# Kernel tuning notes

Hardware: AMD Instinct MI355X
Metric: run time of the kernel (lower is better)

The kernel has to match this reference:

```python
import jax, jax.numpy as jnp
import numpy as np

D_MODEL = 1024
N_HEADS = 16
HEAD_DIM = D_MODEL // N_HEADS
NEG_INF = -1e30


def _rotary(v):
    # v: [B, H, T, hd]. Original module rotates each (even, odd) pair by 90 deg:
    # out[..., 2i] = -v[..., 2i+1]; out[..., 2i+1] = v[..., 2i]
    v2 = v.reshape(*v.shape[:-1], HEAD_DIM // 2, 2)
    return jnp.stack([-v2[..., 1], v2[..., 0]], axis=-1).reshape(v.shape)


def setup_inputs() -> dict:
    key = jax.random.key(0)
    ks = jax.random.split(key, 9)
    B, T, D = 2, 2048, D_MODEL
    s = 1.0 / np.sqrt(D)
    inp = {
        "x": jax.random.normal(ks[0], (B, T, D), dtype=jnp.float32),
        "Wq_w": jax.random.normal(ks[1], (D, D), dtype=jnp.float32) * s,
        "Wq_b": jnp.zeros((D,), dtype=jnp.float32),
        "Wk_w": jax.random.normal(ks[2], (D, D), dtype=jnp.float32) * s,
        "Wk_b": jnp.zeros((D,), dtype=jnp.float32),
        "Wv_w": jax.random.normal(ks[3], (D, D), dtype=jnp.float32) * s,
        "Wv_b": jnp.zeros((D,), dtype=jnp.float32),
        "Wo_w": jax.random.normal(ks[4], (D, D), dtype=jnp.float32) * s,
        "Wo_b": jnp.zeros((D,), dtype=jnp.float32),
    }
    # create_sparse_mask: block-diagonal True windows of size T//4
    window = T // 4
    blk = jnp.arange(T) // window
    inp["sparse_mask"] = blk[:, None] == blk[None, :]
    return inp


def reference(x, Wq_w, Wq_b, Wk_w, Wk_b, Wv_w, Wv_b, Wo_w, Wo_b, sparse_mask):
    B, T, D = x.shape
    H, hd = N_HEADS, HEAD_DIM

    def proj(w, b):  # [B,T,D] -> [B,H,T,hd]
        return (x @ w.T + b).reshape(B, T, H, hd).transpose(0, 2, 1, 3)

    q = _rotary(proj(Wq_w, Wq_b))
    k = _rotary(proj(Wk_w, Wk_b))
    v = proj(Wv_w, Wv_b)

    scores = jnp.einsum("bhqd,bhkd->bhqk", q, k) / jnp.sqrt(jnp.asarray(hd, x.dtype))
    causal = jnp.tril(jnp.ones((T, T), dtype=bool))
    allowed = sparse_mask & causal  # block-diagonal AND causal
    scores = jnp.where(allowed, scores, NEG_INF)
    attn = jax.nn.softmax(scores, axis=-1)  # dropout_p=0.1 omitted (eval mode)
    out = jnp.einsum("bhqk,bhkd->bhqd", attn, v)
    out = out.transpose(0, 2, 1, 3).reshape(B, T, D)
    return out @ Wo_w.T + Wo_b
```

## Files before the change

### kernel.cpp

```cpp
#include <hip/hip_runtime.h>
#include <hip/hip_bf16.h>
#include <stdint.h>

typedef __attribute__((ext_vector_type(4))) float f32x4;
typedef __attribute__((ext_vector_type(8))) __bf16 bf16x8;
typedef __attribute__((ext_vector_type(4))) unsigned short u16x4;
typedef __attribute__((ext_vector_type(8))) unsigned short u16x8;
typedef const __attribute__((address_space(1))) void* as1_cvp;
typedef __attribute__((address_space(3))) void* as3_vp;

#define LOG2E 1.44269504088896340736f

#define VMW0() asm volatile("s_waitcnt vmcnt(0)" ::: "memory")
#define VMW2() asm volatile("s_waitcnt vmcnt(2)" ::: "memory")
#define VMW4() asm volatile("s_waitcnt vmcnt(4)" ::: "memory")
#define BAR()  do { __builtin_amdgcn_sched_barrier(0); __builtin_amdgcn_s_barrier(); \
                    __builtin_amdgcn_sched_barrier(0); } while (0)

static __device__ __forceinline__ unsigned short f2bf(float f) {
  union { float f; unsigned int u; } c; c.f = f;
  unsigned int r = c.u + 0x7FFFu + ((c.u >> 16) & 1u);
  return (unsigned short)(r >> 16);
}

static __device__ __forceinline__ void gl_lds16(const void* g, void* l) {
  __builtin_amdgcn_global_load_lds((as1_cvp)(uintptr_t)g, (as3_vp)(uintptr_t)l, 16, 0, 0);
}

__global__ __launch_bounds__(256) void cvt_kernel(
    const float* __restrict__ x, const float* __restrict__ wq, const float* __restrict__ wk,
    const float* __restrict__ wv, const float* __restrict__ wo,
    unsigned short* __restrict__ xb, unsigned short* __restrict__ wqb,
    unsigned short* __restrict__ wkb, unsigned short* __restrict__ wvb,
    unsigned short* __restrict__ wob) {
  long e = ((long)blockIdx.x * 256 + threadIdx.x) * 8;
  const float* s; unsigned short* d; long o;
  if (e < 4194304)      { s = x;  d = xb;  o = e; }
  else if (e < 5242880) { s = wq; d = wqb; o = e - 4194304; }
  else if (e < 6291456) { s = wk; d = wkb; o = e - 5242880; }
  else if (e < 7340032) { s = wv; d = wvb; o = e - 6291456; }
  else                  { s = wo; d = wob; o = e - 7340032; }
  float4 a = *(const float4*)(s + o);
  float4 b = *(const float4*)(s + o + 4);
  u16x8 v;
  v[0] = f2bf(a.x); v[1] = f2bf(a.y); v[2] = f2bf(a.z); v[3] = f2bf(a.w);
  v[4] = f2bf(b.x); v[5] = f2bf(b.y); v[6] = f2bf(b.z); v[7] = f2bf(b.w);
  *(u16x8*)(d + o) = v;
}

__global__ __launch_bounds__(512, 2) void gemm_qkv8(
    const unsigned short* __restrict__ xb, const unsigned short* __restrict__ wcat,
    const float* __restrict__ bq, const float* __restrict__ bk, const float* __restrict__ bv,
    unsigned short* __restrict__ qo, unsigned short* __restrict__ ko,
    unsigned short* __restrict__ vto) {
  __shared__ __align__(16) char lds[114688];
  const int tid = threadIdx.x;
  const int lane = tid & 63, wid = tid >> 6;
  const int wm = wid >> 1, wn = wid & 1;
  const int c = lane & 15, g = lane >> 4;

  const int bid = blockIdx.x;
  const int xcd = bid & 7, idx = bid >> 3;
  const int m0 = (((xcd >> 1) << 2) + (idx >> 3)) << 8;
  const int n0 = (((xcd & 1) << 3) + (idx & 7)) * 192;

  const int srow = tid >> 3;
  const int coff = (((tid & 7) ^ (srow & 7)) << 4);
  const char* Ab = (const char*)xb;
  const char* Bb = (const char*)wcat;

  const int swzr0 = ((g ^ (c & 7)) << 4);
  const int swzr1 = (((4 | g) ^ (c & 7)) << 4);

  f32x4 acc[4][6] = {};

  auto STAGE = [&](int kt, int unit) {
    char* db = lds + (kt & 1) * 57344;
    const char* gp; char* dst;
    if (unit < 3) {
      gp = Bb + ((long)(n0 + unit * 64 + srow) << 11) + (kt << 7) + coff;
      dst = db + 32768 + unit * 8192 + tid * 16;
    } else {
      const int u = unit - 3;
      gp = Ab + ((long)(m0 + u * 64 + srow) << 11) + (kt << 7) + coff;
      dst = db + u * 8192 + tid * 16;
    }
    gl_lds16(gp, dst);
  };

#pragma unroll
  for (int uu = 0; uu < 7; ++uu) STAGE(0, uu);
  VMW0();
  BAR();

#pragma unroll 1
  for (int kt = 0; kt < 16; ++kt) {
    const int bufb = (kt & 1) * 57344;
    if (kt < 15) {
#pragma unroll
      for (int uu = 0; uu < 7; ++uu) STAGE(kt + 1, uu);
    }
    bf16x8 aa[4][2];
    const char* pA = lds + bufb + (wm << 13) + (c << 7);
#pragma unroll
    for (int f = 0; f < 4; ++f) {
      aa[f][0] = *(const bf16x8*)(pA + (f << 11) + swzr0);
      aa[f][1] = *(const bf16x8*)(pA + (f << 11) + swzr1);
    }
#pragma unroll
    for (int nf = 0; nf < 6; ++nf) {
      const int rB = wn * 96 + (nf << 4) + c;
      const char* pB = lds + bufb + 32768 + ((rB >> 6) << 13) + ((rB & 63) << 7);
      bf16x8 b0 = *(const bf16x8*)(pB + swzr0);
      bf16x8 b1 = *(const bf16x8*)(pB + swzr1);
      __builtin_amdgcn_s_setprio(1);
#pragma unroll
      for (int f = 0; f < 4; ++f)
        acc[f][nf] = __builtin_amdgcn_mfma_f32_16x16x32_bf16(aa[f][0], b0, acc[f][nf], 0, 0, 0);
#pragma unroll
      for (int f = 0; f < 4; ++f)
        acc[f][nf] = __builtin_amdgcn_mfma_f32_16x16x32_bf16(aa[f][1], b1, acc[f][nf], 0, 0, 0);
      __builtin_amdgcn_s_setprio(0);
    }
    if (kt < 15) VMW0();
    BAR();
  }

#pragma unroll
  for (int nf = 0; nf < 6; ++nf) {
    const int n = n0 + wn * 96 + (nf << 4) + c;
    const int z = n >> 10, nn = n & 1023;
    const float bb_ = (z == 0 ? bq : z == 1 ? bk : bv)[nn];
    const float sc = (z == 0) ? 0.125f : 1.0f;
    const int h = nn >> 6, dd = nn & 63;
#pragma unroll
    for (int a = 0; a < 4; ++a) {
      const int mb = m0 + (wm << 6) + (a << 4) + (g << 2);
      const int b = mb >> 11, tt = mb & 2047;
      if (z < 2) {
        unsigned short* dst = (z == 0 ? qo : ko) +
            ((((long)(b << 4) + h) << 11) + tt) * 64 + dd;
#pragma unroll
        for (int j = 0; j < 4; ++j) dst[(long)j * 64] = f2bf((acc[a][nf][j] + bb_) * sc);
      } else {
        u16x4 pk;
#pragma unroll
        for (int j = 0; j < 4; ++j) pk[j] = f2bf(acc[a][nf][j] + bb_);
        *(u16x4*)(vto + ((((long)((b << 4) + h) << 6) + dd) << 11) + tt) = pk;
      }
    }
  }
}

__global__ __launch_bounds__(512, 2) void gemm_oproj8(
    const unsigned short* __restrict__ ab, const unsigned short* __restrict__ wob,
    const float* __restrict__ bo, float* __restrict__ out) {
  __shared__ __align__(16) char lds[65536];
  const int tid = threadIdx.x;
  const int lane = tid & 63, wid = tid >> 6;
  const int wm = wid >> 2, wn = wid & 3;
  const int c = lane & 15, g = lane >> 4;

  const int bid = blockIdx.x;
  const int swz = (bid & 7) * 32 + (bid >> 3);
  const int n0 = (swz & 7) << 7;
  const int m0 = (swz >> 3) << 7;

  const int srow = tid >> 3;
  const int coff = (((tid & 7) ^ (srow & 7)) << 4);
  const char* Ab = (const char*)ab;
  const char* Bb = (const char*)wob;

  const int swzr0 = ((g ^ (c & 7)) << 4);
  const int swzr1 = (((4 | g) ^ (c & 7)) << 4);

  f32x4 acc[4][2] = {};
  bf16x8 afrA[2][2], afrB[2][2], bbf[2][2];

  auto STAGE = [&](int kt, int unit) {
    char* db = lds + (kt & 1) * 32768;
    const char* gp;
    if (unit < 2) gp = Ab + ((long)(m0 + unit * 64 + srow) << 11) + (kt << 7) + coff;
    else          gp = Bb + ((long)(n0 + (unit - 2) * 64 + srow) << 11) + (kt << 7) + coff;
    gl_lds16(gp, db + unit * 8192 + tid * 16);
  };
  auto RDA = [&](bf16x8 (&dst)[2][2], int bufb, int u) {
    const char* p = lds + bufb + (((u << 6) + (wm << 5) + c) << 7);
#pragma unroll
    for (int f = 0; f < 2; ++f) {
      dst[f][0] = *(const bf16x8*)(p + (f << 11) + swzr0);
      dst[f][1] = *(const bf16x8*)(p + (f << 11) + swzr1);
    }
  };
  auto RDB = [&](int bufb) {
#pragma unroll
    for (int nf = 0; nf < 2; ++nf) {
      const char* p = lds + bufb + 16384 + (((nf << 6) + (wn << 4) + c) << 7);
      bbf[nf][0] = *(const bf16x8*)(p + swzr0);
      bbf[nf][1] = *(const bf16x8*)(p + swzr1);
    }
  };
  auto MM = [&](int u, const bf16x8 (&af)[2][2]) {
    __builtin_amdgcn_s_setprio(1);
#pragma unroll
    for (int f = 0; f < 2; ++f)
#pragma unroll
      for (int nf = 0; nf < 2; ++nf)
#pragma unroll
        for (int kf = 0; kf < 2; ++kf)
          acc[u * 2 + f][nf] = __builtin_amdgcn_mfma_f32_16x16x32_bf16(
              af[f][kf], bbf[nf][kf], acc[u * 2 + f][nf], 0, 0, 0);
    __builtin_amdgcn_s_setprio(0);
  };

  STAGE(0, 0); STAGE(0, 2); STAGE(0, 3); STAGE(0, 1);

#pragma unroll 1
  for (int kt = 0; kt < 15; ++kt) {
    const int bufb = (kt & 1) * 32768;
    STAGE(kt + 1, 0); STAGE(kt + 1, 2);
    VMW2(); BAR();
    RDB(bufb); RDA(afrA, bufb, 0); RDA(afrB, bufb, 1);
    MM(0, afrA);
    STAGE(kt + 1, 3); STAGE(kt + 1, 1);
    BAR();
    MM(1, afrB);
  }
  {
    VMW0(); BAR();
    RDB(32768); RDA(afrA, 32768, 0); RDA(afrB, 32768, 1);
    MM(0, afrA);
    MM(1, afrB);
  }

#pragma unroll
  for (int nf = 0; nf < 2; ++nf) {
    const int n = n0 + (nf << 6) + (wn << 4) + c;
    const float bb = bo[n];
#pragma unroll
    for (int a = 0; a < 4; ++a) {
      const int mb = m0 + ((a >> 1) << 6) + (wm << 5) + ((a & 1) << 4) + (g << 2);
#pragma unroll
      for (int j = 0; j < 4; ++j)
        out[((long)(mb + j) << 10) + n] = acc[a][nf][j] + bb;
    }
  }
}

__global__ __launch_bounds__(512) void attn_kernel(
    const unsigned short* __restrict__ qg, const unsigned short* __restrict__ kg,
    const unsigned short* __restrict__ vtg, unsigned short* __restrict__ og) {
  __shared__ __align__(16) char kv_s[3][16384];
  __shared__ __align__(16) char p_s[8][2304];

  const int bx = blockIdx.x, bh = blockIdx.y;
  const int qt = ((bx & 3) << 2) + 3 - (bx >> 2);
  const int tid = threadIdx.x;
  const int lane = tid & 63, w = tid >> 6;
  const int c = lane & 15, g = lane >> 4;
  const int q0 = qt << 7;
  const int wstart = q0 & ~511;
  const int nt = ((q0 - wstart) >> 6) + 2;

  const unsigned short* qrow = qg + (((long)bh << 11) + q0 + (w << 4) + c) * 64;
  bf16x8 qa0 = *(const bf16x8*)(qrow + (g << 3));
  bf16x8 qa1 = *(const bf16x8*)(qrow + (g << 3) + 32);

  float m_run = -3.0e38f, l_run = 0.0f;
  f32x4 oacc[4] = {};

  const int sr = tid >> 3;
  const int jx16 = (((tid & 7) ^ (sr & 7)) << 4);
  const char* kbase = (const char*)kg + ((((long)bh << 11) + sr) << 7) + jx16;
  const char* vbase = (const char*)vtg + ((((long)bh << 6) + sr) << 12) + jx16;
  const int t16 = tid << 4;

  auto STAGEKV = [&](int kv0, int bsel) {
    char* dst = kv_s[bsel];
    gl_lds16(kbase + ((long)kv0 << 7), dst + t16);
    gl_lds16(vbase + ((long)kv0 << 1), dst + 8192 + t16);
  };

  STAGEKV(wstart, 0);
  STAGEKV(wstart + 64, 1);

  int rsel = 0, ssel = 2;
  for (int t = 0; t < nt; ++t) {
    if (t + 2 < nt) {
      STAGEKV(wstart + ((t + 2) << 6), ssel);
      VMW4();
    } else if (t + 1 < nt) {
      VMW2();
    } else {
      VMW0();
    }
    BAR();

    const char* kb_ = kv_s[rsel];
    const char* vb_ = kv_s[rsel] + 8192;
    const int kv0 = wstart + (t << 6);

    f32x4 sacc[4] = {};
    __builtin_amdgcn_s_setprio(1);
#pragma unroll
    for (int mf = 0; mf < 4; ++mf) {
      const int kr = (mf << 4) + c;
      const char* kp = kb_ + (kr << 7);
      bf16x8 k0 = *(const bf16x8*)(kp + ((g ^ (kr & 7)) << 4));
      bf16x8 k1 = *(const bf16x8*)(kp + (((4 | g) ^ (kr & 7)) << 4));
      sacc[mf] = __builtin_amdgcn_mfma_f32_16x16x32_bf16(k0, qa0, sacc[mf], 0, 0, 0);
      sacc[mf] = __builtin_amdgcn_mfma_f32_16x16x32_bf16(k1, qa1, sacc[mf], 0, 0, 0);
    }
    __builtin_amdgcn_s_setprio(0);

    const int dkv = kv0 - q0;
    if (dkv > (w << 4) - 64) {
      const int qrel = (w << 4) + c;
#pragma unroll
      for (int mf = 0; mf < 4; ++mf)
#pragma unroll
        for (int j = 0; j < 4; ++j)
          if (dkv + (mf << 4) + (g << 2) + j > qrel) sacc[mf][j] = -3.0e38f;
    }

    float pmax = -3.0e38f;
#pragma unroll
    for (int mf = 0; mf < 4; ++mf)
#pragma unroll
      for (int j = 0; j < 4; ++j) pmax = fmaxf(pmax, sacc[mf][j]);
    pmax = fmaxf(pmax, __shfl_xor(pmax, 16));
    pmax = fmaxf(pmax, __shfl_xor(pmax, 32));

    const bool resc = !__all(pmax <= m_run + 8.0f);
    const float m_new = resc ? fmaxf(m_run, pmax) : m_run;

    float lsum = 0.0f;
#pragma unroll
    for (int mf = 0; mf < 4; ++mf)
#pragma unroll
      for (int j = 0; j < 4; ++j) {
        const float p = __builtin_amdgcn_exp2f((sacc[mf][j] - m_new) * LOG2E);
        sacc[mf][j] = p;
        lsum += p;
      }
    lsum += __shfl_xor(lsum, 16);
    lsum += __shfl_xor(lsum, 32);

    if (resc) {
      const float alpha = __builtin_amdgcn_exp2f((m_run - m_new) * LOG2E);
      l_run *= alpha;
#pragma unroll
      for (int j = 0; j < 4; ++j) {
        const float aj = __shfl(alpha, (g << 2) + j);
#pragma unroll
        for (int nf = 0; nf < 4; ++nf) oacc[nf][j] *= aj;
      }
      m_run = m_new;
    }
    l_run += lsum;

    {
      char* pw = p_s[w] + c * 144;
#pragma unroll
      for (int mf = 0; mf < 4; ++mf) {
        u16x4 pk;
#pragma unroll
        for (int j = 0; j < 4; ++j) pk[j] = f2bf(sacc[mf][j]);
        *(u16x4*)(pw + (mf << 5) + (g << 3)) = pk;
      }
    }

    const char* pr = p_s[w] + c * 144;
    __builtin_amdgcn_s_setprio(1);
#pragma unroll
    for (int kk = 0; kk < 2; ++kk) {
      bf16x8 pa = *(const bf16x8*)(pr + (kk << 6) + (g << 4));
#pragma unroll
      for (int nf = 0; nf < 4; ++nf) {
        const int vr = (nf << 4) + c;
        bf16x8 vb = *(const bf16x8*)(vb_ + (vr << 7) +
                                     ((((kk << 2) | g) ^ (vr & 7)) << 4));
        oacc[nf] = __builtin_amdgcn_mfma_f32_16x16x32_bf16(pa, vb, oacc[nf], 0, 0, 0);
      }
    }
    __builtin_amdgcn_s_setprio(0);
    BAR();

    rsel = (rsel == 2) ? 0 : rsel + 1;
    ssel = (ssel == 2) ? 0 : ssel + 1;
  }

  const int b = bh >> 4, h = bh & 15;
#pragma unroll
  for (int j = 0; j < 4; ++j) {
    const float linv = 1.0f / __shfl(l_run, (g << 2) + j);
    const int trow = q0 + (w << 4) + (g << 2) + j;
    unsigned short* dst = og + ((((long)(b << 11)) + trow) << 10) + (h << 6);
#pragma unroll
    for (int nf = 0; nf < 4; ++nf)
      dst[(nf << 4) + c] = f2bf(oacc[nf][j] * linv);
  }
}

extern "C" void kernel_launch(void* const* d_in, const int* in_sizes, int n_in,
                              void* d_out, int out_size, void* d_ws, size_t ws_size,
                              hipStream_t stream) {
  const float* x  = (const float*)d_in[0];
  const float* wq = (const float*)d_in[1];
  const float* bq = (const float*)d_in[2];
  const float* wk = (const float*)d_in[3];
  const float* bk = (const float*)d_in[4];
  const float* wv = (const float*)d_in[5];
  const float* bv = (const float*)d_in[6];
  const float* wo = (const float*)d_in[7];
  const float* bo = (const float*)d_in[8];

  char* ws = (char*)d_ws;
  unsigned short* xb    = (unsigned short*)(ws);
  unsigned short* wqb   = (unsigned short*)(ws + 8388608);
  unsigned short* wkb   = (unsigned short*)(ws + 10485760);
  unsigned short* wvb   = (unsigned short*)(ws + 12582912);
  unsigned short* wob   = (unsigned short*)(ws + 14680064);
  unsigned short* qb    = (unsigned short*)(ws + 16777216);
  unsigned short* kb    = (unsigned short*)(ws + 25165824);
  unsigned short* vtb   = (unsigned short*)(ws + 33554432);
  unsigned short* attnb = xb;

  cvt_kernel<<<4096, 256, 0, stream>>>(x, wq, wk, wv, wo, xb, wqb, wkb, wvb, wob);
  gemm_qkv8<<<256, 512, 0, stream>>>(xb, wqb, bq, bk, bv, qb, kb, vtb);
  attn_kernel<<<dim3(16, 32), 512, 0, stream>>>(qb, kb, vtb, attnb);
  gemm_oproj8<<<256, 512, 0, stream>>>(attnb, wob, bo, (float*)d_out);
}
```

Measured before the change: 79.01 us.

## Reorder q-tile scheduling per head and tighten softmax arithmetic with packed bf16 converts

Swaps the block-to-query-tile mapping for table lookups that differ between the first and second half of batch-heads, so heavy and light causal tiles are spread differently. The softmax max and sum reductions become tree-shaped, and the exponent argument is computed with a single FMA using a prescaled max. Manual round-to-nearest bf16 conversion is replaced by the hardware v_cvt_pk_bf16_f32 instruction, which packs two values per instruction. Together these aim to cut VALU work in the inner loop and improve load balance. The mapping tables may sit in scratch memory, and exp2 of FMA differs slightly in rounding from the original.

```diff
diff --git a/kernel.cpp b/kernel.cpp
--- a/kernel.cpp
+++ b/kernel.cpp
@@ -6,6 +6,7 @@
 typedef __attribute__((ext_vector_type(8))) __bf16 bf16x8;
 typedef __attribute__((ext_vector_type(4))) unsigned short u16x4;
 typedef __attribute__((ext_vector_type(8))) unsigned short u16x8;
+typedef __attribute__((ext_vector_type(2))) unsigned int u32x2;
 typedef const __attribute__((address_space(1))) void* as1_cvp;
 typedef __attribute__((address_space(3))) void* as3_vp;
 
@@ -254,7 +255,9 @@
   __shared__ __align__(16) char p_s[8][2304];
 
   const int bx = blockIdx.x, bh = blockIdx.y;
-  const int qt = ((bx & 3) << 2) + 3 - (bx >> 2);
+  const int map1[16] = {3,7,11,15, 2,6,10,14, 0,4,8,12, 1,5,9,13};
+  const int map2[16] = {0,4,8,12, 1,5,9,13, 3,7,11,15, 2,6,10,14};
+  const int qt = (bh < 16) ? map1[bx] : map2[bx];
   const int tid = threadIdx.x;
   const int lane = tid & 63, w = tid >> 6;
   const int c = lane & 15, g = lane >> 4;
@@ -323,26 +326,29 @@
           if (dkv + (mf << 4) + (g << 2) + j > qrel) sacc[mf][j] = -3.0e38f;
     }
 
-    float pmax = -3.0e38f;
+    float pm[4];
 #pragma unroll
     for (int mf = 0; mf < 4; ++mf)
-#pragma unroll
-      for (int j = 0; j < 4; ++j) pmax = fmaxf(pmax, sacc[mf][j]);
+      pm[mf] = fmaxf(fmaxf(sacc[mf][0], sacc[mf][1]), fmaxf(sacc[mf][2], sacc[mf][3]));
+    float pmax = fmaxf(fmaxf(pm[0], pm[1]), fmaxf(pm[2], pm[3]));
     pmax = fmaxf(pmax, __shfl_xor(pmax, 16));
     pmax = fmaxf(pmax, __shfl_xor(pmax, 32));
 
     const bool resc = !__all(pmax <= m_run + 8.0f);
     const float m_new = resc ? fmaxf(m_run, pmax) : m_run;
 
-    float lsum = 0.0f;
-#pragma unroll
-    for (int mf = 0; mf < 4; ++mf)
-#pragma unroll
-      for (int j = 0; j < 4; ++j) {
-        const float p = __builtin_amdgcn_exp2f((sacc[mf][j] - m_new) * LOG2E);
-        sacc[mf][j] = p;
-        lsum += p;
-      }
+    const float mL = m_new * LOG2E;
+    float ls[4];
+#pragma unroll
+    for (int mf = 0; mf < 4; ++mf) {
+      float p0 = __builtin_amdgcn_exp2f(__builtin_fmaf(sacc[mf][0], LOG2E, -mL));
+      float p1 = __builtin_amdgcn_exp2f(__builtin_fmaf(sacc[mf][1], LOG2E, -mL));
+      float p2 = __builtin_amdgcn_exp2f(__builtin_fmaf(sacc[mf][2], LOG2E, -mL));
+      float p3 = __builtin_amdgcn_exp2f(__builtin_fmaf(sacc[mf][3], LOG2E, -mL));
+      sacc[mf][0] = p0; sacc[mf][1] = p1; sacc[mf][2] = p2; sacc[mf][3] = p3;
+      ls[mf] = (p0 + p1) + (p2 + p3);
+    }
+    float lsum = (ls[0] + ls[1]) + (ls[2] + ls[3]);
     lsum += __shfl_xor(lsum, 16);
     lsum += __shfl_xor(lsum, 32);
 
@@ -363,10 +369,11 @@
       char* pw = p_s[w] + c * 144;
 #pragma unroll
       for (int mf = 0; mf < 4; ++mf) {
-        u16x4 pk;
-#pragma unroll
-        for (int j = 0; j < 4; ++j) pk[j] = f2bf(sacc[mf][j]);
-        *(u16x4*)(pw + (mf << 5) + (g << 3)) = pk;
+        unsigned int p01, p23;
+        asm("v_cvt_pk_bf16_f32 %0, %1, %2" : "=v"(p01) : "v"(sacc[mf][0]), "v"(sacc[mf][1]));
+        asm("v_cvt_pk_bf16_f32 %0, %1, %2" : "=v"(p23) : "v"(sacc[mf][2]), "v"(sacc[mf][3]));
+        u32x2 pk; pk[0] = p01; pk[1] = p23;
+        *(u32x2*)(pw + (mf << 5) + (g << 3)) = pk;
       }
     }
 
```

Measured after the change: 77.98 us. About the same (-1.3%).
